# Kernel optimization log

Measured on AMD Instinct MI355X. Metric: run time of the kernel, lower is better.

The kernel has to match this reference:

```python
import jax, jax.numpy as jnp
import numpy as np
import math

B, H, S, D = 4, 8, 512, 64

def setup_inputs() -> dict:
    key = jax.random.key(0)
    k1, k2, k3, k4, k5 = jax.random.split(key, 5)
    return {
        "query": jax.random.normal(k1, (B, H, S, D), dtype=jnp.float32),
        "key": jax.random.normal(k2, (B, H, S, D), dtype=jnp.float32),
        "value": jax.random.normal(k3, (B, H, S, D), dtype=jnp.float32),
        "relem": jax.random.normal(k4, (B, S, S, D), dtype=jnp.float32),
        "mask": jax.random.randint(k5, (B, S), 0, 2, dtype=jnp.int32),
    }

def reference(query, key, value, relem, mask):
    d = query.shape[-1]
    # relscore[b,h,s,t] = sum_d q[b,h,s,d] * relem[b,s,t,d]
    relscore = jnp.einsum("bhsd,bstd->bhst", query, relem)
    scores = jnp.einsum("bhsd,bhtd->bhst", query, key)
    scores = (relscore + scores) / math.sqrt(d)
    # mask [B,S] -> [B,1,S,S] (broadcast of key mask over query positions)
    m = mask[:, None, None, :]  # repeat over query dim is a broadcast
    scores = jnp.where(m == 0, jnp.float32(-1e9), scores)
    p_attn = jax.nn.softmax(scores, axis=-1)
    ans1 = jnp.einsum("bhst,bhtd->bhsd", p_attn, value)
    ans2 = jnp.einsum("bhst,bstd->bhsd", p_attn, relem)
    return ans1 + ans2, p_attn
```

## Files before the change

### kernel.cpp

```cpp
#include <hip/hip_runtime.h>


typedef __attribute__((ext_vector_type(8))) short short8;
typedef __attribute__((ext_vector_type(4))) float f32x4;

#define MFMA16(a, b, c) __builtin_amdgcn_mfma_f32_16x16x32_bf16(a, b, c, 0, 0, 0)

__device__ __forceinline__ unsigned short f2bf(float x) {
  unsigned int u = __float_as_uint(x);
  u += 0x7fffu + ((u >> 16) & 1u);
  return (unsigned short)(u >> 16);
}
__device__ __forceinline__ float bf2f(unsigned int s) {
  return __uint_as_float(s << 16);
}
__device__ __forceinline__ short8 pack8(const float4& a, const float4& b) {
  short8 r;
  r[0] = (short)f2bf(a.x); r[1] = (short)f2bf(a.y);
  r[2] = (short)f2bf(a.z); r[3] = (short)f2bf(a.w);
  r[4] = (short)f2bf(b.x); r[5] = (short)f2bf(b.y);
  r[6] = (short)f2bf(b.z); r[7] = (short)f2bf(b.w);
  return r;
}
__device__ __forceinline__ int RLI(int t, int d) {
  return ((t << 6) | d) ^ ((((t & 7) ^ ((t >> 3) & 7))) << 3);
}
__device__ __forceinline__ int SBI(int h, int t) {
  return ((h << 9) | t) ^ ((h & 7) << 3);
}

template <bool WSK>
__global__ __launch_bounds__(256, 4)
void qk_mfma(const float* __restrict__ Q, const float* __restrict__ K,
             void* __restrict__ skout) {
  const int bh   = blockIdx.x >> 6;
  const int tile = blockIdx.x & 63;
  const int s0 = (tile >> 3) << 6;
  const int t0 = (tile & 7) << 6;
  const int w    = threadIdx.x >> 6;
  const int lane = threadIdx.x & 63;
  const int rrow = lane & 15;
  const int kg   = lane >> 4;

  const float* Qb = Q + ((size_t)bh << 15);
  const float* Kb = K + ((size_t)bh << 15);

  const float* qp = Qb + (((s0 + (w << 4) + rrow) << 6) + (kg << 3));
  const short8 a0 = pack8(*reinterpret_cast<const float4*>(qp),
                          *reinterpret_cast<const float4*>(qp + 4));
  const short8 a1 = pack8(*reinterpret_cast<const float4*>(qp + 32),
                          *reinterpret_cast<const float4*>(qp + 36));

  float4 b0, b1, b2, b3;
  {
    const float* kp = Kb + (((t0 + rrow) << 6) + (kg << 3));
    b0 = *reinterpret_cast<const float4*>(kp);
    b1 = *reinterpret_cast<const float4*>(kp + 4);
    b2 = *reinterpret_cast<const float4*>(kp + 32);
    b3 = *reinterpret_cast<const float4*>(kp + 36);
  }
#pragma unroll
  for (int nt = 0; nt < 4; ++nt) {
    const short8 bb0 = pack8(b0, b1);
    const short8 bb1 = pack8(b2, b3);
    if (nt < 3) {
      const float* kp = Kb + (((t0 + ((nt + 1) << 4) + rrow) << 6) + (kg << 3));
      b0 = *reinterpret_cast<const float4*>(kp);
      b1 = *reinterpret_cast<const float4*>(kp + 4);
      b2 = *reinterpret_cast<const float4*>(kp + 32);
      b3 = *reinterpret_cast<const float4*>(kp + 36);
    }
    f32x4 c = {0.0f, 0.0f, 0.0f, 0.0f};
    c = MFMA16(a0, bb0, c);
    c = MFMA16(a1, bb1, c);
    const int tcol = t0 + (nt << 4) + rrow;
    const int srow = s0 + (w << 4) + (kg << 2);
    if constexpr (WSK) {
      unsigned short* ob = (unsigned short*)skout + ((size_t)bh << 18);
#pragma unroll
      for (int r = 0; r < 4; ++r)
        ob[(size_t)(srow + r) * 512 + tcol] = f2bf(c[r]);
    } else {
      float* ob = (float*)skout + ((size_t)bh << 18);
#pragma unroll
      for (int r = 0; r < 4; ++r)
        ob[(size_t)(srow + r) * 512 + tcol] = c[r];
    }
  }
}

template <bool WSK>
__global__ __launch_bounds__(256, 2)
void attn_v7k(const float* __restrict__ Q, const float* __restrict__ R,
              const int* __restrict__ Mk, float* __restrict__ ans,
              float* __restrict__ pout, const void* __restrict__ skin) {
  __shared__ __align__(16) unsigned short smem[8 * 512 + 512 * 64];
  unsigned short* Sb = smem;
  unsigned short* Rl = smem + 8 * 512;

  const int tid = threadIdx.x;
  const int b = blockIdx.x >> 9;
  const int s = blockIdx.x & 511;
  const int bh0 = b << 3;

  const float* Rg = R + ((size_t)((b << 9) + s) << 15);

  {
    const int c16 = tid & 15;
    const int r0  = tid >> 4;
#pragma unroll
    for (int pg = 0; pg < 4; ++pg) {
      float4 tmp[8];
#pragma unroll
      for (int j = 0; j < 8; ++j) {
        const int t = (((pg << 3) + j) << 4) + r0;
        tmp[j] = *reinterpret_cast<const float4*>(Rg + (t << 6) + (c16 << 2));
      }
#pragma unroll
      for (int j = 0; j < 8; ++j) {
        const int t = (((pg << 3) + j) << 4) + r0;
        unsigned short* dst = &Rl[RLI(t, c16 << 2)];
        dst[0] = f2bf(tmp[j].x); dst[1] = f2bf(tmp[j].y);
        dst[2] = f2bf(tmp[j].z); dst[3] = f2bf(tmp[j].w);
      }
    }
  }
  __syncthreads();

  const int lane = tid & 63;
  const int w    = tid >> 6;
  const int nn   = lane & 15;
  const int kg   = lane >> 4;

  {
    const int hq = nn & 7;
    const float* Qg = Q + ((size_t)(((bh0 + hq) << 9) + s) << 6);
    const short8 aq0 = pack8(*reinterpret_cast<const float4*>(Qg + (kg << 3)),
                             *reinterpret_cast<const float4*>(Qg + (kg << 3) + 4));
    const short8 aq1 = pack8(*reinterpret_cast<const float4*>(Qg + 32 + (kg << 3)),
                             *reinterpret_cast<const float4*>(Qg + 36 + (kg << 3)));

#pragma unroll
    for (int i = 0; i < 8; ++i) {
      const int t0 = ((w << 3) + i) << 4;
      const short8 bb0 = *reinterpret_cast<const short8*>(&Rl[RLI(t0 + nn, kg << 3)]);
      const short8 bb1 = *reinterpret_cast<const short8*>(&Rl[RLI(t0 + nn, 32 + (kg << 3))]);
      f32x4 c = {0.0f, 0.0f, 0.0f, 0.0f};
      c = MFMA16(aq0, bb0, c);
      c = MFMA16(aq1, bb1, c);
      if (kg < 2) {
#pragma unroll
        for (int r = 0; r < 4; ++r)
          Sb[SBI((kg << 2) + r, t0 + nn)] = f2bf(c[r]);
      }
    }
  }
  __syncthreads();

  {
    float bias[8];
#pragma unroll
    for (int k = 0; k < 8; ++k)
      bias[k] = Mk[(b << 9) + lane + (k << 6)] ? 0.0f : -1.0e9f;

#pragma unroll
    for (int rr = 0; rr < 2; ++rr) {
      const int h = (w << 1) + rr;
      float* po = pout + ((size_t)(bh0 + h) << 18) + ((size_t)s << 9);
      const unsigned short* skw =
          WSK ? (const unsigned short*)skin + ((size_t)(bh0 + h) << 18) + ((size_t)s << 9)
              : nullptr;
      const float* skf =
          WSK ? nullptr
              : (const float*)skin + ((size_t)(bh0 + h) << 18) + ((size_t)s << 9);

      float v[8];
#pragma unroll
      for (int k = 0; k < 8; ++k) {
        const int t = lane + (k << 6);
        const float skv = WSK ? bf2f((unsigned int)skw[t]) : skf[t];
        v[k] = (bf2f((unsigned int)Sb[SBI(h, t)]) + skv) * 0.125f + bias[k];
      }
      float m = v[0];
#pragma unroll
      for (int k = 1; k < 8; ++k) m = fmaxf(m, v[k]);
      m = fmaxf(m, __shfl_xor(m, 1));
      m = fmaxf(m, __shfl_xor(m, 2));
      m = fmaxf(m, __shfl_xor(m, 4));
      m = fmaxf(m, __shfl_xor(m, 8));
      m = fmaxf(m, __shfl_xor(m, 16));
      m = fmaxf(m, __shfl_xor(m, 32));

      float e[8], ss = 0.0f;
#pragma unroll
      for (int k = 0; k < 8; ++k) { e[k] = __expf(v[k] - m); ss += e[k]; }
      ss += __shfl_xor(ss, 1);
      ss += __shfl_xor(ss, 2);
      ss += __shfl_xor(ss, 4);
      ss += __shfl_xor(ss, 8);
      ss += __shfl_xor(ss, 16);
      ss += __shfl_xor(ss, 32);
      const float inv = 1.0f / ss;

#pragma unroll
      for (int k = 0; k < 8; ++k) {
        const float p = e[k] * inv;
        const int t = lane + (k << 6);
        po[t] = p;
        Sb[SBI(h, t)] = f2bf(p);
      }
    }
  }
  __syncthreads();

  {
    const int n0 = w << 4;
    f32x4 acc = {0.0f, 0.0f, 0.0f, 0.0f};
#pragma unroll
    for (int ks = 0; ks < 16; ++ks) {
      const int tb = (ks << 5) + (kg << 3);
      const short8 af = *reinterpret_cast<const short8*>(&Sb[SBI(nn, tb)]);
      short8 bf;
#pragma unroll
      for (int j = 0; j < 8; ++j)
        bf[j] = (short)Rl[RLI(tb + j, n0 + nn)];
      acc = MFMA16(af, bf, acc);
    }
    if (kg < 2) {
#pragma unroll
      for (int r = 0; r < 4; ++r) {
        const int h = (kg << 2) + r;
        ans[((size_t)(((bh0 + h) << 9) + s) << 6) + n0 + nn] = acc[r];
      }
    }
  }
}

__global__ __launch_bounds__(256, 2)
void pv_mfma(const float* __restrict__ V, const float* __restrict__ pout,
             float* __restrict__ ans) {
  __shared__ __align__(16) unsigned short Vl[512 * 64];

  const int tid = threadIdx.x;
  const int bh = blockIdx.x >> 4;
  const int s0 = (blockIdx.x & 15) << 5;

  const float* Vg = V + ((size_t)bh << 15);
  {
    const int c16 = tid & 15;
    const int r0  = tid >> 4;
#pragma unroll
    for (int pg = 0; pg < 4; ++pg) {
      float4 tmp[8];
#pragma unroll
      for (int j = 0; j < 8; ++j) {
        const int t = (((pg << 3) + j) << 4) + r0;
        tmp[j] = *reinterpret_cast<const float4*>(Vg + (t << 6) + (c16 << 2));
      }
#pragma unroll
      for (int j = 0; j < 8; ++j) {
        const int t = (((pg << 3) + j) << 4) + r0;
        unsigned short* dst = &Vl[RLI(t, c16 << 2)];
        dst[0] = f2bf(tmp[j].x); dst[1] = f2bf(tmp[j].y);
        dst[2] = f2bf(tmp[j].z); dst[3] = f2bf(tmp[j].w);
      }
    }
  }
  __syncthreads();

  const int lane = tid & 63;
  const int w    = tid >> 6;
  const int nn   = lane & 15;
  const int kg   = lane >> 4;
  const int rw   = w & 1;
  const int ch   = w >> 1;
  const int srow = s0 + (rw << 4) + nn;

  const float* Pg = pout + ((size_t)bh << 18) + ((size_t)srow << 9);

  f32x4 acc0 = {0.f, 0.f, 0.f, 0.f}, acc1 = acc0;

  float4 pa = *reinterpret_cast<const float4*>(Pg + (kg << 3));
  float4 pb = *reinterpret_cast<const float4*>(Pg + (kg << 3) + 4);
#pragma unroll
  for (int ks = 0; ks < 16; ++ks) {
    const short8 af = pack8(pa, pb);
    if (ks < 15) {
      pa = *reinterpret_cast<const float4*>(Pg + ((ks + 1) << 5) + (kg << 3));
      pb = *reinterpret_cast<const float4*>(Pg + ((ks + 1) << 5) + (kg << 3) + 4);
    }
    const int tb = (ks << 5) + (kg << 3);
    short8 b0, b1;
#pragma unroll
    for (int j = 0; j < 8; ++j) {
      b0[j] = (short)Vl[RLI(tb + j, (ch << 5) + nn)];
      b1[j] = (short)Vl[RLI(tb + j, (ch << 5) + 16 + nn)];
    }
    acc0 = MFMA16(af, b0, acc0);
    acc1 = MFMA16(af, b1, acc1);
  }

  {
    const int sb = s0 + (rw << 4) + (kg << 2);
#pragma unroll
    for (int r = 0; r < 4; ++r) {
      float* ap = ans + ((size_t)bh << 15) + ((size_t)(sb + r) << 6) + (ch << 5) + nn;
      ap[0]  += acc0[r];
      ap[16] += acc1[r];
    }
  }
}

extern "C" void kernel_launch(void* const* d_in, const int* in_sizes, int n_in,
                              void* d_out, int out_size, void* d_ws, size_t ws_size,
                              hipStream_t stream) {
  const float* Q  = (const float*)d_in[0];
  const float* K  = (const float*)d_in[1];
  const float* V  = (const float*)d_in[2];
  const float* R  = (const float*)d_in[3];
  const int*   Mk = (const int*)d_in[4];
  float* ans  = (float*)d_out;
  float* pout = ans + (size_t)4 * 8 * 512 * 64;
  (void)in_sizes; (void)n_in; (void)out_size;

  const size_t sk_bf16_bytes = (size_t)4 * 8 * 512 * 512 * 2;

  if (ws_size >= sk_bf16_bytes) {
    hipLaunchKernelGGL((qk_mfma<true>), dim3(2048), dim3(256), 0, stream,
                       Q, K, d_ws);
    hipLaunchKernelGGL((attn_v7k<true>), dim3(2048), dim3(256), 0, stream,
                       Q, R, Mk, ans, pout, d_ws);
  } else {
    hipLaunchKernelGGL((qk_mfma<false>), dim3(2048), dim3(256), 0, stream,
                       Q, K, pout);
    hipLaunchKernelGGL((attn_v7k<false>), dim3(2048), dim3(256), 0, stream,
                       Q, R, Mk, ans, pout, pout);
  }
  hipLaunchKernelGGL(pv_mfma, dim3(512), dim3(256), 0, stream, V, pout, ans);
}
```

Baseline: 113.9 us.

## Double threads per block in attention and PV kernels with split-K reduction

Raises the block size of the relative-attention kernel and the PV kernel from 256 to 512 threads. Each wave now handles one head's softmax instead of two, and the P·R product is split across two wave halves along the key axis, with partial sums reduced through a small shared buffer. The PV kernel gives each wave one 16-column tile instead of two. The goal is more waves in flight per block to hide global-load and LDS latency, at the cost of an extra barrier, a shared-memory reduction, and fewer independent MFMAs per wave.

```diff
diff --git a/kernel.cpp b/kernel.cpp
--- a/kernel.cpp
+++ b/kernel.cpp
@@ -90,11 +90,12 @@
 }
 
 template <bool WSK>
-__global__ __launch_bounds__(256, 2)
-void attn_v7k(const float* __restrict__ Q, const float* __restrict__ R,
-              const int* __restrict__ Mk, float* __restrict__ ans,
-              float* __restrict__ pout, const void* __restrict__ skin) {
+__global__ __launch_bounds__(512, 4)
+void attn_v8(const float* __restrict__ Q, const float* __restrict__ R,
+             const int* __restrict__ Mk, float* __restrict__ ans,
+             float* __restrict__ pout, const void* __restrict__ skin) {
   __shared__ __align__(16) unsigned short smem[8 * 512 + 512 * 64];
+  __shared__ __align__(16) float Pp[4][8][16];
   unsigned short* Sb = smem;
   unsigned short* Rl = smem + 8 * 512;
 
@@ -106,20 +107,20 @@
   const float* Rg = R + ((size_t)((b << 9) + s) << 15);
 
   {
-    const int c16 = tid & 15;
-    const int r0  = tid >> 4;
-#pragma unroll
-    for (int pg = 0; pg < 4; ++pg) {
+    const int d4 = tid & 15;
+    const int tr = tid >> 4;
+#pragma unroll
+    for (int pg = 0; pg < 2; ++pg) {
       float4 tmp[8];
 #pragma unroll
       for (int j = 0; j < 8; ++j) {
-        const int t = (((pg << 3) + j) << 4) + r0;
-        tmp[j] = *reinterpret_cast<const float4*>(Rg + (t << 6) + (c16 << 2));
+        const int t = (pg << 8) + (j << 5) + tr;
+        tmp[j] = *reinterpret_cast<const float4*>(Rg + (t << 6) + (d4 << 2));
       }
 #pragma unroll
       for (int j = 0; j < 8; ++j) {
-        const int t = (((pg << 3) + j) << 4) + r0;
-        unsigned short* dst = &Rl[RLI(t, c16 << 2)];
+        const int t = (pg << 8) + (j << 5) + tr;
+        unsigned short* dst = &Rl[RLI(t, d4 << 2)];
         dst[0] = f2bf(tmp[j].x); dst[1] = f2bf(tmp[j].y);
         dst[2] = f2bf(tmp[j].z); dst[3] = f2bf(tmp[j].w);
       }
@@ -141,8 +142,8 @@
                              *reinterpret_cast<const float4*>(Qg + 36 + (kg << 3)));
 
 #pragma unroll
-    for (int i = 0; i < 8; ++i) {
-      const int t0 = ((w << 3) + i) << 4;
+    for (int i = 0; i < 4; ++i) {
+      const int t0 = ((w << 2) + i) << 4;
       const short8 bb0 = *reinterpret_cast<const short8*>(&Rl[RLI(t0 + nn, kg << 3)]);
       const short8 bb1 = *reinterpret_cast<const short8*>(&Rl[RLI(t0 + nn, 32 + (kg << 3))]);
       f32x4 c = {0.0f, 0.0f, 0.0f, 0.0f};
@@ -158,67 +159,67 @@
   __syncthreads();
 
   {
+    const int h = w;
     float bias[8];
 #pragma unroll
     for (int k = 0; k < 8; ++k)
       bias[k] = Mk[(b << 9) + lane + (k << 6)] ? 0.0f : -1.0e9f;
 
-#pragma unroll
-    for (int rr = 0; rr < 2; ++rr) {
-      const int h = (w << 1) + rr;
-      float* po = pout + ((size_t)(bh0 + h) << 18) + ((size_t)s << 9);
-      const unsigned short* skw =
-          WSK ? (const unsigned short*)skin + ((size_t)(bh0 + h) << 18) + ((size_t)s << 9)
-              : nullptr;
-      const float* skf =
-          WSK ? nullptr
-              : (const float*)skin + ((size_t)(bh0 + h) << 18) + ((size_t)s << 9);
-
-      float v[8];
-#pragma unroll
-      for (int k = 0; k < 8; ++k) {
-        const int t = lane + (k << 6);
-        const float skv = WSK ? bf2f((unsigned int)skw[t]) : skf[t];
-        v[k] = (bf2f((unsigned int)Sb[SBI(h, t)]) + skv) * 0.125f + bias[k];
-      }
-      float m = v[0];
-#pragma unroll
-      for (int k = 1; k < 8; ++k) m = fmaxf(m, v[k]);
-      m = fmaxf(m, __shfl_xor(m, 1));
-      m = fmaxf(m, __shfl_xor(m, 2));
-      m = fmaxf(m, __shfl_xor(m, 4));
-      m = fmaxf(m, __shfl_xor(m, 8));
-      m = fmaxf(m, __shfl_xor(m, 16));
-      m = fmaxf(m, __shfl_xor(m, 32));
-
-      float e[8], ss = 0.0f;
-#pragma unroll
-      for (int k = 0; k < 8; ++k) { e[k] = __expf(v[k] - m); ss += e[k]; }
-      ss += __shfl_xor(ss, 1);
-      ss += __shfl_xor(ss, 2);
-      ss += __shfl_xor(ss, 4);
-      ss += __shfl_xor(ss, 8);
-      ss += __shfl_xor(ss, 16);
-      ss += __shfl_xor(ss, 32);
-      const float inv = 1.0f / ss;
-
-#pragma unroll
-      for (int k = 0; k < 8; ++k) {
-        const float p = e[k] * inv;
-        const int t = lane + (k << 6);
-        po[t] = p;
-        Sb[SBI(h, t)] = f2bf(p);
-      }
+    float* po = pout + ((size_t)(bh0 + h) << 18) + ((size_t)s << 9);
+    const unsigned short* skw =
+        WSK ? (const unsigned short*)skin + ((size_t)(bh0 + h) << 18) + ((size_t)s << 9)
+            : nullptr;
+    const float* skf =
+        WSK ? nullptr
+            : (const float*)skin + ((size_t)(bh0 + h) << 18) + ((size_t)s << 9);
+
+    float v[8];
+#pragma unroll
+    for (int k = 0; k < 8; ++k) {
+      const int t = lane + (k << 6);
+      const float skv = WSK ? bf2f((unsigned int)skw[t]) : skf[t];
+      v[k] = (bf2f((unsigned int)Sb[SBI(h, t)]) + skv) * 0.125f + bias[k];
+    }
+    float m = v[0];
+#pragma unroll
+    for (int k = 1; k < 8; ++k) m = fmaxf(m, v[k]);
+    m = fmaxf(m, __shfl_xor(m, 1));
+    m = fmaxf(m, __shfl_xor(m, 2));
+    m = fmaxf(m, __shfl_xor(m, 4));
+    m = fmaxf(m, __shfl_xor(m, 8));
+    m = fmaxf(m, __shfl_xor(m, 16));
+    m = fmaxf(m, __shfl_xor(m, 32));
+
+    float e[8], ss = 0.0f;
+#pragma unroll
+    for (int k = 0; k < 8; ++k) { e[k] = __expf(v[k] - m); ss += e[k]; }
+    ss += __shfl_xor(ss, 1);
+    ss += __shfl_xor(ss, 2);
+    ss += __shfl_xor(ss, 4);
+    ss += __shfl_xor(ss, 8);
+    ss += __shfl_xor(ss, 16);
+    ss += __shfl_xor(ss, 32);
+    const float inv = 1.0f / ss;
+
+#pragma unroll
+    for (int k = 0; k < 8; ++k) {
+      const float p = e[k] * inv;
+      const int t = lane + (k << 6);
+      po[t] = p;
+      Sb[SBI(h, t)] = f2bf(p);
     }
   }
   __syncthreads();
 
   {
-    const int n0 = w << 4;
+    const int dt = w & 3;
+    const int kh = w >> 2;
+    const int n0 = dt << 4;
+
     f32x4 acc = {0.0f, 0.0f, 0.0f, 0.0f};
 #pragma unroll
-    for (int ks = 0; ks < 16; ++ks) {
-      const int tb = (ks << 5) + (kg << 3);
+    for (int k8 = 0; k8 < 8; ++k8) {
+      const int tb = (((kh << 3) + k8) << 5) + (kg << 3);
       const short8 af = *reinterpret_cast<const short8*>(&Sb[SBI(nn, tb)]);
       short8 bf;
 #pragma unroll
@@ -226,17 +227,24 @@
         bf[j] = (short)Rl[RLI(tb + j, n0 + nn)];
       acc = MFMA16(af, bf, acc);
     }
-    if (kg < 2) {
+    if (kh == 1 && kg < 2) {
+#pragma unroll
+      for (int r = 0; r < 4; ++r)
+        Pp[dt][(kg << 2) + r][nn] = acc[r];
+    }
+    __syncthreads();
+    if (kh == 0 && kg < 2) {
 #pragma unroll
       for (int r = 0; r < 4; ++r) {
         const int h = (kg << 2) + r;
-        ans[((size_t)(((bh0 + h) << 9) + s) << 6) + n0 + nn] = acc[r];
-      }
-    }
-  }
-}
-
-__global__ __launch_bounds__(256, 2)
+        ans[((size_t)(((bh0 + h) << 9) + s) << 6) + n0 + nn] =
+            acc[r] + Pp[dt][h][nn];
+      }
+    }
+  }
+}
+
+__global__ __launch_bounds__(512, 4)
 void pv_mfma(const float* __restrict__ V, const float* __restrict__ pout,
              float* __restrict__ ans) {
   __shared__ __align__(16) unsigned short Vl[512 * 64];
@@ -247,20 +255,20 @@
 
   const float* Vg = V + ((size_t)bh << 15);
   {
-    const int c16 = tid & 15;
-    const int r0  = tid >> 4;
-#pragma unroll
-    for (int pg = 0; pg < 4; ++pg) {
+    const int d4 = tid & 15;
+    const int tr = tid >> 4;
+#pragma unroll
+    for (int pg = 0; pg < 2; ++pg) {
       float4 tmp[8];
 #pragma unroll
       for (int j = 0; j < 8; ++j) {
-        const int t = (((pg << 3) + j) << 4) + r0;
-        tmp[j] = *reinterpret_cast<const float4*>(Vg + (t << 6) + (c16 << 2));
+        const int t = (pg << 8) + (j << 5) + tr;
+        tmp[j] = *reinterpret_cast<const float4*>(Vg + (t << 6) + (d4 << 2));
       }
 #pragma unroll
       for (int j = 0; j < 8; ++j) {
-        const int t = (((pg << 3) + j) << 4) + r0;
-        unsigned short* dst = &Vl[RLI(t, c16 << 2)];
+        const int t = (pg << 8) + (j << 5) + tr;
+        unsigned short* dst = &Vl[RLI(t, d4 << 2)];
         dst[0] = f2bf(tmp[j].x); dst[1] = f2bf(tmp[j].y);
         dst[2] = f2bf(tmp[j].z); dst[3] = f2bf(tmp[j].w);
       }
@@ -273,12 +281,13 @@
   const int nn   = lane & 15;
   const int kg   = lane >> 4;
   const int rw   = w & 1;
-  const int ch   = w >> 1;
+  const int cq   = w >> 1;
+  const int n0   = cq << 4;
   const int srow = s0 + (rw << 4) + nn;
 
   const float* Pg = pout + ((size_t)bh << 18) + ((size_t)srow << 9);
 
-  f32x4 acc0 = {0.f, 0.f, 0.f, 0.f}, acc1 = acc0;
+  f32x4 acc = {0.f, 0.f, 0.f, 0.f};
 
   float4 pa = *reinterpret_cast<const float4*>(Pg + (kg << 3));
   float4 pb = *reinterpret_cast<const float4*>(Pg + (kg << 3) + 4);
@@ -290,23 +299,19 @@
       pb = *reinterpret_cast<const float4*>(Pg + ((ks + 1) << 5) + (kg << 3) + 4);
     }
     const int tb = (ks << 5) + (kg << 3);
-    short8 b0, b1;
-#pragma unroll
-    for (int j = 0; j < 8; ++j) {
-      b0[j] = (short)Vl[RLI(tb + j, (ch << 5) + nn)];
-      b1[j] = (short)Vl[RLI(tb + j, (ch << 5) + 16 + nn)];
-    }
-    acc0 = MFMA16(af, b0, acc0);
-    acc1 = MFMA16(af, b1, acc1);
+    short8 bf;
+#pragma unroll
+    for (int j = 0; j < 8; ++j)
+      bf[j] = (short)Vl[RLI(tb + j, n0 + nn)];
+    acc = MFMA16(af, bf, acc);
   }
 
   {
     const int sb = s0 + (rw << 4) + (kg << 2);
 #pragma unroll
     for (int r = 0; r < 4; ++r) {
-      float* ap = ans + ((size_t)bh << 15) + ((size_t)(sb + r) << 6) + (ch << 5) + nn;
-      ap[0]  += acc0[r];
-      ap[16] += acc1[r];
+      float* ap = ans + ((size_t)bh << 15) + ((size_t)(sb + r) << 6) + n0 + nn;
+      ap[0] += acc[r];
     }
   }
 }
@@ -328,13 +333,13 @@
   if (ws_size >= sk_bf16_bytes) {
     hipLaunchKernelGGL((qk_mfma<true>), dim3(2048), dim3(256), 0, stream,
                        Q, K, d_ws);
-    hipLaunchKernelGGL((attn_v7k<true>), dim3(2048), dim3(256), 0, stream,
+    hipLaunchKernelGGL((attn_v8<true>), dim3(2048), dim3(512), 0, stream,
                        Q, R, Mk, ans, pout, d_ws);
   } else {
     hipLaunchKernelGGL((qk_mfma<false>), dim3(2048), dim3(256), 0, stream,
                        Q, K, pout);
-    hipLaunchKernelGGL((attn_v7k<false>), dim3(2048), dim3(256), 0, stream,
+    hipLaunchKernelGGL((attn_v8<false>), dim3(2048), dim3(512), 0, stream,
                        Q, R, Mk, ans, pout, pout);
   }
-  hipLaunchKernelGGL(pv_mfma, dim3(512), dim3(256), 0, stream, V, pout, ans);
-}
+  hipLaunchKernelGGL(pv_mfma, dim3(512), dim3(512), 0, stream, V, pout, ans);
+}
```

New measurement: 111.5 us. 2.1% less time.
